# Kernel tuning notes

Measured on AMD Instinct MI355X. Metric: run time of the kernel, lower is better.

Reference implementation:

```python
import jax, jax.numpy as jnp
import numpy as np

B, T, N, D = 256, 200, 8, 64
MODEL = N * D          # 512
FFN_H = 1024 * N // 4  # 2048
EPS = 1.1920929e-07    # torch.finfo(float32).eps (nn.RMSNorm default eps=None)


def setup_inputs() -> dict:
    key = jax.random.key(0)
    ks = jax.random.split(key, 9)
    def xavier(k, shape):
        fan_in, fan_out = shape[-2], shape[-1]
        lim = float(np.sqrt(6.0 / (fan_in + fan_out)))
        return jax.random.uniform(k, shape, jnp.float32, -lim, lim)
    q = jax.random.normal(ks[0], (B, N, D), jnp.float32)
    seq = jax.random.normal(ks[1], (B, T, MODEL), jnp.float32)
    seq_mask = jax.random.randint(ks[2], (B, T), 0, 2) > 0
    seq_mask = seq_mask.at[:, 0].set(True)  # ensure >=1 valid position per row
    return {
        "q": q,
        "seq": seq,
        "rms_w": jnp.ones((MODEL,), jnp.float32),
        "w1": xavier(ks[3], (MODEL, FFN_H)),
        "w2": xavier(ks[4], (MODEL, FFN_H)),
        "w3": xavier(ks[5], (FFN_H, MODEL)),
        "w_k": xavier(ks[6], (N, D, D)),
        "w_v": xavier(ks[7], (N, D, D)),
        "seq_mask": seq_mask,
    }


def reference(q, seq, rms_w, w1, w2, w3, w_k, w_v, seq_mask):
    # RMSNorm
    sn = seq * jax.lax.rsqrt(jnp.mean(seq * seq, axis=-1, keepdims=True) + EPS) * rms_w
    # SwiGLU FFN + residual (dropout=0 / eval)
    h = (jax.nn.silu(sn @ w1) * (sn @ w2)) @ w3 + seq  # (B,T,N*D)
    hh = h.reshape(B, T, N, D)
    keys = jnp.einsum('btnd,nde->bnte', hh, w_k)    # (B,N,T,D)
    values = jnp.einsum('btnd,nde->bnte', hh, w_v)  # (B,N,T,D)
    scale = D ** (-0.5)
    scores = jnp.einsum('bnd,bntd->bnt', q, keys) * scale  # single-query attention
    scores = jnp.where(seq_mask[:, None, :], scores, -jnp.inf)
    attn = jax.nn.softmax(scores, axis=-1)
    ctx = jnp.einsum('bnt,bntd->bnd', attn, values)
    return ctx + q
```

## Files before the change

kernel.cpp:

```cpp
#include <hip/hip_runtime.h>
#include <hip/hip_fp16.h>
#include <cstdint>
#include <cstddef>

typedef unsigned short u16t;
typedef __bf16 bf16x8 __attribute__((ext_vector_type(8)));
typedef float f32x4 __attribute__((ext_vector_type(4)));
typedef unsigned short u16x8 __attribute__((ext_vector_type(8)));

#define BT_ROWS 51200
#define MODEL 512
#define FFNH 2048

__device__ __forceinline__ float bf2f(u16t u) {
  union { unsigned int i; float f; } v; v.i = ((unsigned int)u) << 16; return v.f;
}
__device__ __forceinline__ u16t f2bf(float f) {
  union { float f; unsigned int i; } v; v.f = f;
  return (u16t)((v.i + 0x7fffu + ((v.i >> 16) & 1u)) >> 16);
}
__device__ __forceinline__ float ldf(const void* p, size_t i, int dt) {
  if (dt == 1) return ((const float*)p)[i];
  u16t u = ((const u16t*)p)[i];
  if (dt == 0) return bf2f(u);
  __half h; *(u16t*)&h = u; return __half2float(h);
}
__device__ __forceinline__ void stf(void* p, size_t i, int dt, float f) {
  if (dt == 1) { ((float*)p)[i] = f; }
  else if (dt == 0) { ((u16t*)p)[i] = f2bf(f); }
  else { __half h = __float2half(f); ((u16t*)p)[i] = *(u16t*)&h; }
}
__device__ __forceinline__ void gl2lds16(const void* g, void* l) {
  __builtin_amdgcn_global_load_lds((const __attribute__((address_space(1))) void*)g,
                                   (__attribute__((address_space(3))) void*)l, 16, 0, 0);
}

__global__ __launch_bounds__(256) void detect_dtype_k(const unsigned int* __restrict__ w1,
                                                      int* __restrict__ dflag) {
  __shared__ int sh[8];
  int a = 0, bc = 0;
  for (int it = 0; it < 64; it++) {
    unsigned int w = w1[it * 256 + threadIdx.x];
    u16t lo = (u16t)(w & 0xffffu), hi = (u16t)(w >> 16);
    float flo = bf2f(lo);
    a += (!(fabsf(flo) < 0.25f)) ? 1 : 0;
    __half hh; *(u16t*)&hh = hi; float fhi = __half2float(hh);
    bc += (fabsf(fhi) > 0.25f && fabsf(fhi) < 256.f) ? 1 : 0;
  }
#pragma unroll
  for (int o = 32; o; o >>= 1) { a += __shfl_xor(a, o); bc += __shfl_xor(bc, o); }
  int w = threadIdx.x >> 6;
  if ((threadIdx.x & 63) == 0) { sh[w] = a; sh[4 + w] = bc; }
  __syncthreads();
  if (threadIdx.x == 0) {
    int A = sh[0] + sh[1] + sh[2] + sh[3];
    int B = sh[4] + sh[5] + sh[6] + sh[7];
    dflag[0] = (A > 256) ? 1 : ((B < 256) ? 2 : 0);
  }
}

__global__ __launch_bounds__(256) void detect_mask_k(const unsigned int* __restrict__ msk,
                                                     int* __restrict__ flag) {
  int i = blockIdx.x * 256 + threadIdx.x;
  int bad = 0;
  if (i < 12800) bad = (msk[i] > 1u) ? 1 : 0;
  unsigned long long bl = __ballot(bad);
  if ((threadIdx.x & 63) == 0 && bl) atomicOr(flag, 1);
}

__global__ __launch_bounds__(256) void rmsnorm_k(const void* __restrict__ seq,
                                                 const void* __restrict__ w,
                                                 const int* __restrict__ dfp,
                                                 u16t* __restrict__ xn) {
  const int dt = dfp[0];
  int row = blockIdx.x * 4 + (threadIdx.x >> 6);
  int lane = threadIdx.x & 63;
  size_t base = (size_t)row * MODEL + lane * 8;
  float x[8]; float ss = 0.f;
  if (dt == 0) {
    u16x8 xv = *(const u16x8*)((const u16t*)seq + base);
#pragma unroll
    for (int j = 0; j < 8; j++) { x[j] = bf2f(xv[j]); ss += x[j] * x[j]; }
  } else if (dt == 1) {
    const f32x4* p = (const f32x4*)((const float*)seq + base);
    f32x4 va = p[0], vb = p[1];
#pragma unroll
    for (int j = 0; j < 4; j++) { x[j] = va[j]; x[4 + j] = vb[j]; }
#pragma unroll
    for (int j = 0; j < 8; j++) ss += x[j] * x[j];
  } else {
#pragma unroll
    for (int j = 0; j < 8; j++) { x[j] = ldf(seq, base + j, dt); ss += x[j] * x[j]; }
  }
#pragma unroll
  for (int o = 32; o; o >>= 1) ss += __shfl_xor(ss, o);
  float rstd = rsqrtf(ss * (1.f / 512.f) + 1.1920929e-07f);
  u16x8 ov;
#pragma unroll
  for (int j = 0; j < 8; j++) ov[j] = f2bf(x[j] * rstd * ldf(w, lane * 8 + j, dt));
  *(u16x8*)(xn + base) = ov;
}

__global__ __launch_bounds__(256) void transpose_k(const void* __restrict__ src,
                                                   u16t* __restrict__ dst,
                                                   const int* __restrict__ dfp,
                                                   int R, int C, int ih) {
  const int dt = dfp[0];
  __shared__ u16t tile[32][33];
  int x = threadIdx.x & 31, y = threadIdx.x >> 5;
  int c0 = blockIdx.x * 32, r0 = blockIdx.y * 32;
#pragma unroll
  for (int i = 0; i < 32; i += 8)
    tile[y + i][x] = f2bf(ldf(src, (size_t)(r0 + y + i) * C + c0 + x, dt));
  __syncthreads();
#pragma unroll
  for (int i = 0; i < 32; i += 8) {
    int n = c0 + y + i;
    int vr = (ih >= 0) ? (((n >> 4) << 5) + ih * 16 + (n & 15)) : n;
    dst[(size_t)vr * R + r0 + x] = tile[x][y + i];
  }
}


#define FENCE_BAR()                              \
  do {                                           \
    __builtin_amdgcn_sched_barrier(0);           \
    __builtin_amdgcn_s_barrier();                \
    __builtin_amdgcn_sched_barrier(0);           \
  } while (0)

#define MM16(afr, bfr, MHc, NHc)                                                    \
  do {                                                                              \
    __builtin_amdgcn_s_setprio(1);                                                  \
    _Pragma("unroll") for (int ks_ = 0; ks_ < 2; ks_++)                             \
        _Pragma("unroll") for (int mi_ = 0; mi_ < 4; mi_++)                         \
            _Pragma("unroll") for (int ni_ = 0; ni_ < 2; ni_++)                     \
                acc[(MHc)*4 + mi_][(NHc)*2 + ni_] =                                 \
                    __builtin_amdgcn_mfma_f32_16x16x32_bf16(                        \
                        afr[mi_][ks_], bfr[ni_][ks_],                               \
                        acc[(MHc)*4 + mi_][(NHc)*2 + ni_], 0, 0, 0);                \
    __builtin_amdgcn_s_setprio(0);                                                  \
  } while (0)

template <int K>
__device__ __forceinline__ void gemm256_core(const u16t* __restrict__ Ag,
                                             const u16t* __restrict__ Bg,
                                             u16t* __restrict__ As,
                                             u16t* __restrict__ Bs,
                                             f32x4 (&acc)[8][4]) {
  constexpr int NKT = K / 64;
  const int tid = threadIdx.x;
  const int lane = tid & 63;
  const int wave = tid >> 6;
  const int wr = wave >> 2, wc = wave & 3;
  const int quad = lane >> 4, l16 = lane & 15;
  const int wu = tid & ~63;

  auto stage = [&](const u16t* __restrict__ G, u16t* __restrict__ L, int s, int h) {
#pragma unroll
    for (int c = 0; c < 2; c++) {
      int chunk = c * 512 + tid;
      int r = chunk >> 3;
      int k8 = (chunk & 7) ^ (r & 7);
      gl2lds16(G + (size_t)(h * 128 + r) * K + s * 64 + k8 * 8,
               L + (s & 1) * 16384 + h * 8192 + (size_t)(c * 512 + wu) * 8);
    }
  };
  auto lda = [&](bf16x8(&a)[4][2], int u, int MH) {
    const u16t* S = As + (u & 1) * 16384;
#pragma unroll
    for (int ks = 0; ks < 2; ks++)
#pragma unroll
      for (int mi = 0; mi < 4; mi++) {
        int row = wr * 128 + MH * 64 + mi * 16 + l16;
        int sw = (ks * 4 + quad) ^ (row & 7);
        a[mi][ks] = *(const bf16x8*)(S + row * 64 + sw * 8);
      }
  };
  auto ldb = [&](bf16x8(&b)[2][2], int u, int NH) {
    const u16t* S = Bs + (u & 1) * 16384;
#pragma unroll
    for (int ks = 0; ks < 2; ks++)
#pragma unroll
      for (int ni = 0; ni < 2; ni++) {
        int row = wc * 64 + NH * 32 + ni * 16 + l16;
        int sw = (ks * 4 + quad) ^ (row & 7);
        b[ni][ks] = *(const bf16x8*)(S + row * 64 + sw * 8);
      }
  };

  bf16x8 a[4][2], b0[2][2], b1[2][2];

  stage(Ag, As, 0, 0);
  stage(Ag, As, 0, 1);
  stage(Bg, Bs, 0, 0);
  stage(Bg, Bs, 0, 1);
  if (NKT > 1) stage(Ag, As, 1, 0);
  __builtin_amdgcn_sched_barrier(0);
  if (NKT > 1) asm volatile("s_waitcnt vmcnt(2)" ::: "memory");
  else         asm volatile("s_waitcnt vmcnt(0)" ::: "memory");
  __builtin_amdgcn_s_barrier();
  __builtin_amdgcn_sched_barrier(0);

  for (int u = 0; u < NKT; u++) {
    lda(a, u, 0);
    ldb(b0, u, 0);
    if (u + 1 < NKT) stage(Ag, As, u + 1, 1);
    FENCE_BAR();
    MM16(a, b0, 0, 0);
    FENCE_BAR();
    ldb(b1, u, 1);
    if (u + 1 < NKT) stage(Bg, Bs, u + 1, 0);
    FENCE_BAR();
    MM16(a, b1, 0, 1);
    FENCE_BAR();
    lda(a, u, 1);
    if (u + 1 < NKT) stage(Bg, Bs, u + 1, 1);
    FENCE_BAR();
    MM16(a, b0, 1, 0);
    FENCE_BAR();
    if (u + 2 < NKT) stage(Ag, As, u + 2, 0);
    FENCE_BAR();
    MM16(a, b1, 1, 1);
    __builtin_amdgcn_sched_barrier(0);
    if (u < NKT - 2)       asm volatile("s_waitcnt vmcnt(2)" ::: "memory");
    else if (u == NKT - 2) asm volatile("s_waitcnt vmcnt(0)" ::: "memory");
    __builtin_amdgcn_s_barrier();
    __builtin_amdgcn_sched_barrier(0);
  }
}

__device__ __forceinline__ int xcd_swz(int o, int nwg) {
  int q = nwg >> 3, r = nwg & 7;
  int xcd = o & 7, i = o >> 3;
  return (xcd < r ? xcd * (q + 1) : r * (q + 1) + (xcd - r) * q) + i;
}

__global__ __launch_bounds__(512, 2) void ffn_gemm1(const u16t* __restrict__ Xn,
                                                    const u16t* __restrict__ W12t,
                                                    u16t* __restrict__ Act) {
  __shared__ u16t As[2 * 16384];
  __shared__ u16t Bs[2 * 16384];
  const int tid = threadIdx.x;
  const int lane = tid & 63;
  const int wave = tid >> 6;
  const int wr = wave >> 2, wc = wave & 3;
  const int quad = lane >> 4, l16 = lane & 15;

  int o = blockIdx.y * 16 + blockIdx.x;
  int s = xcd_swz(o, gridDim.y * 16);
  int bx = s & 15, by = s >> 4;

  f32x4 acc[8][4];
  const f32x4 zf = {0.f, 0.f, 0.f, 0.f};
#pragma unroll
  for (int m = 0; m < 8; m++)
#pragma unroll
    for (int n = 0; n < 4; n++) acc[m][n] = zf;

  gemm256_core<512>(Xn + (size_t)by * 256 * 512, W12t + (size_t)bx * 256 * 512, As, Bs, acc);

  const int mBase = by * 256;
#pragma unroll
  for (int mi = 0; mi < 8; mi++)
#pragma unroll
    for (int p = 0; p < 2; p++)
#pragma unroll
      for (int r = 0; r < 4; r++) {
        int row = mBase + wr * 128 + mi * 16 + quad * 4 + r;
        int col = bx * 128 + (wc * 2 + p) * 16 + l16;
        float g1 = acc[mi][2 * p][r], g2 = acc[mi][2 * p + 1][r];
        float sl = g1 / (1.f + __expf(-g1));
        Act[(size_t)row * FFNH + col] = f2bf(sl * g2);
      }
}

__global__ __launch_bounds__(512, 2) void ffn_gemm2(const u16t* __restrict__ Act,
                                                    const u16t* __restrict__ W3t,
                                                    const void* __restrict__ Seq,
                                                    const int* __restrict__ dfp,
                                                    u16t* __restrict__ H, int rowOff) {
  __shared__ u16t As[2 * 16384];
  __shared__ u16t Bs[2 * 16384];
  const int dt = dfp[0];
  const int tid = threadIdx.x;
  const int lane = tid & 63;
  const int wave = tid >> 6;
  const int wr = wave >> 2, wc = wave & 3;
  const int quad = lane >> 4, l16 = lane & 15;

  int o = blockIdx.y * 2 + blockIdx.x;
  int s = xcd_swz(o, gridDim.y * 2);
  int bx = s & 1, by = s >> 1;

  f32x4 acc[8][4];
  const f32x4 zf = {0.f, 0.f, 0.f, 0.f};
#pragma unroll
  for (int m = 0; m < 8; m++)
#pragma unroll
    for (int n = 0; n < 4; n++) acc[m][n] = zf;

  gemm256_core<2048>(Act + (size_t)by * 256 * 2048, W3t + (size_t)bx * 256 * 2048, As, Bs, acc);

  const int mBase = by * 256;
#pragma unroll
  for (int mi = 0; mi < 8; mi++)
#pragma unroll
    for (int ni = 0; ni < 4; ni++)
#pragma unroll
      for (int r = 0; r < 4; r++) {
        int grow = rowOff + mBase + wr * 128 + mi * 16 + quad * 4 + r;
        int col = bx * 256 + wc * 64 + ni * 16 + l16;
        float v = acc[mi][ni][r] + ldf(Seq, (size_t)grow * MODEL + col, dt);
        H[(size_t)grow * MODEL + col] = f2bf(v);
      }
}

__global__ __launch_bounds__(256) void attn_k(const u16t* __restrict__ H,
                                              const void* __restrict__ q,
                                              const void* __restrict__ wk,
                                              const void* __restrict__ wv,
                                              const int* __restrict__ mask,
                                              const int* __restrict__ mflagp,
                                              const int* __restrict__ dfp,
                                              void* __restrict__ out) {
  const int b = blockIdx.x >> 3;
  const int n = blockIdx.x & 7;
  const int tid = threadIdx.x;
  const int w = tid >> 6;
  const int lane = tid & 63;
  const int T = 200;
  const int HS = 66;
  const int dt = dfp[0];
  const int mflag = mflagp[0];

  __shared__ u16t hbuf[200 * HS];
  __shared__ float qk[64];
  __shared__ float sc[200];
  __shared__ float part[256];
  __shared__ float red[8];
  __shared__ float ctx[64];

  for (int chunk = tid; chunk < 1600; chunk += 256) {
    int r = chunk >> 3, c = (chunk & 7) << 3;
    u16x8 v = *(const u16x8*)(H + (size_t)(b * 200 + r) * MODEL + n * 64 + c);
#pragma unroll
    for (int j = 0; j < 8; j++) hbuf[r * HS + c + j] = v[j];
  }

  {
    int d = tid >> 2, sub = tid & 3;
    float s = 0.f;
    size_t wb = ((size_t)n * 64 + d) * 64 + sub * 16;
    size_t qb = (size_t)(b * 8 + n) * 64 + sub * 16;
#pragma unroll
    for (int i = 0; i < 16; i++) s += ldf(wk, wb + i, dt) * ldf(q, qb + i, dt);
    part[tid] = s;
  }
  __syncthreads();
  if (tid < 64) qk[tid] = part[tid * 4] + part[tid * 4 + 1] + part[tid * 4 + 2] + part[tid * 4 + 3];
  __syncthreads();

  float sv = -INFINITY;
  if (tid < T) {
    float s = 0.f;
#pragma unroll 16
    for (int d = 0; d < 64; d++) s += bf2f(hbuf[tid * HS + d]) * qk[d];
    int mv = mflag ? (int)((const unsigned char*)mask)[b * 200 + tid] : mask[b * 200 + tid];
    sv = mv ? s * 0.125f : -INFINITY;
  }

  float mx = sv;
#pragma unroll
  for (int o = 32; o; o >>= 1) mx = fmaxf(mx, __shfl_xor(mx, o));
  if (lane == 0) red[w] = mx;
  __syncthreads();
  float gmax = fmaxf(fmaxf(red[0], red[1]), fmaxf(red[2], red[3]));
  float e = 0.f;
  if (gmax == -INFINITY) {
    if (tid == 0) e = 1.f;
  } else if (tid < T) {
    e = __expf(sv - gmax);
  }
  float s = e;
#pragma unroll
  for (int o = 32; o; o >>= 1) s += __shfl_xor(s, o);
  if (lane == 0) red[4 + w] = s;
  __syncthreads();
  float inv = 1.f / (red[4] + red[5] + red[6] + red[7]);
  if (tid < T) sc[tid] = e * inv;
  __syncthreads();

  float a2 = 0.f;
  for (int t = w; t < T; t += 4) a2 += sc[t] * bf2f(hbuf[t * HS + lane]);
  part[tid] = a2;
  __syncthreads();
  if (tid < 64) ctx[tid] = part[tid] + part[64 + tid] + part[128 + tid] + part[192 + tid];
  __syncthreads();

  {
    int od = tid & 63;
    float s2 = 0.f;
#pragma unroll
    for (int i = 0; i < 16; i++) {
      int d = w * 16 + i;
      s2 += ctx[d] * ldf(wv, ((size_t)n * 64 + d) * 64 + od, dt);
    }
    part[tid] = s2;
  }
  __syncthreads();
  if (tid < 64) {
    size_t oi = (size_t)(b * 8 + n) * 64 + tid;
    stf(out, oi, dt,
        part[tid] + part[64 + tid] + part[128 + tid] + part[192 + tid] + ldf(q, oi, dt));
  }
}

extern "C" void kernel_launch(void* const* d_in, const int* in_sizes, int n_in,
                              void* d_out, int out_size, void* d_ws, size_t ws_size,
                              hipStream_t stream) {
  (void)in_sizes; (void)n_in; (void)out_size;
  const void* q   = d_in[0];
  const void* seq = d_in[1];
  const void* rw  = d_in[2];
  const void* w1  = d_in[3];
  const void* w2  = d_in[4];
  const void* w3  = d_in[5];
  const void* wk  = d_in[6];
  const void* wv  = d_in[7];
  const int*  msk = (const int*)d_in[8];

  char* ws = (char*)d_ws;
  size_t off = 0;
  auto alloc = [&](size_t b) { void* p = ws + off; off = (off + b + 255) & ~(size_t)255; return p; };
  int*  flags = (int*)alloc(512);
  int*  mflag = flags + 0;
  int*  dflag = flags + 4;
  u16t* Xn   = (u16t*)alloc((size_t)BT_ROWS * MODEL * 2);
  u16t* W12t = (u16t*)alloc((size_t)2 * FFNH * MODEL * 2);
  u16t* W3t  = (u16t*)alloc((size_t)MODEL * FFNH * 2);
  size_t actBytes = (ws_size > off) ? (ws_size - off) : 0;
  long ppc = (long)(actBytes / ((size_t)256 * FFNH * 2));
  if (ppc < 1) ppc = 1;
  if (ppc > 100) ppc = 100;
  u16t* ActB = (u16t*)(ws + off);

  hipMemsetAsync(flags, 0, 512, stream);
  detect_dtype_k<<<dim3(1), dim3(256), 0, stream>>>((const unsigned int*)w1, dflag);
  detect_mask_k<<<dim3(50), dim3(256), 0, stream>>>((const unsigned int*)msk, mflag);

  rmsnorm_k<<<dim3(BT_ROWS / 4), dim3(256), 0, stream>>>(seq, rw, dflag, Xn);
  transpose_k<<<dim3(FFNH / 32, MODEL / 32), dim3(256), 0, stream>>>(w1, W12t, dflag, MODEL, FFNH, 0);
  transpose_k<<<dim3(FFNH / 32, MODEL / 32), dim3(256), 0, stream>>>(w2, W12t, dflag, MODEL, FFNH, 1);
  transpose_k<<<dim3(MODEL / 32, FFNH / 32), dim3(256), 0, stream>>>(w3, W3t, dflag, FFNH, MODEL, -1);

  for (int p0 = 0; p0 < 200; p0 += (int)ppc) {
    int panels = (200 - p0 < (int)ppc) ? (200 - p0) : (int)ppc;
    int rows0 = p0 * 256;
    ffn_gemm1<<<dim3(16, panels), dim3(512), 0, stream>>>(
        Xn + (size_t)rows0 * MODEL, W12t, ActB);
    ffn_gemm2<<<dim3(2, panels), dim3(512), 0, stream>>>(
        ActB, W3t, seq, dflag, Xn, rows0);
  }
  attn_k<<<dim3(2048), dim3(256), 0, stream>>>(Xn, q, wk, wv, msk, mflag, dflag, d_out);
}
```

Baseline: 774.7 us.

## Stage whole next K-tile up front and use nontemporal epilogue stores

Replaces the interleaved half-tile staging schedule in the GEMM core with a single issue of the full next K-tile (A and B) at the start of each iteration, followed by a full vmcnt(0) wait at the end. The sched_barrier fences around the mid-iteration barriers are dropped, leaving plain s_barriers. Epilogue stores of the activation and the H output become nontemporal to reduce cache pollution. The simpler schedule removes the finer-grained overlap of loads with MFMAs and waits for all loads each step, and without the sched fences the compiler may move LDS reads across barriers.

Measured after the change: 909.2 us. 1.17x slower.

```diff
diff --git a/kernel.cpp b/kernel.cpp
--- a/kernel.cpp
+++ b/kernel.cpp
@@ -121,13 +121,6 @@
   }
 }
 
-
-#define FENCE_BAR()                              \
-  do {                                           \
-    __builtin_amdgcn_sched_barrier(0);           \
-    __builtin_amdgcn_s_barrier();                \
-    __builtin_amdgcn_sched_barrier(0);           \
-  } while (0)
 
 #define MM16(afr, bfr, MHc, NHc)                                                    \
   do {                                                                              \
@@ -156,14 +149,16 @@
   const int quad = lane >> 4, l16 = lane & 15;
   const int wu = tid & ~63;
 
-  auto stage = [&](const u16t* __restrict__ G, u16t* __restrict__ L, int s, int h) {
-#pragma unroll
-    for (int c = 0; c < 2; c++) {
+  auto stageTile = [&](int s) {
+    u16t* Ad = As + (s & 1) * 16384;
+    u16t* Bd = Bs + (s & 1) * 16384;
+#pragma unroll
+    for (int c = 0; c < 4; c++) {
       int chunk = c * 512 + tid;
       int r = chunk >> 3;
       int k8 = (chunk & 7) ^ (r & 7);
-      gl2lds16(G + (size_t)(h * 128 + r) * K + s * 64 + k8 * 8,
-               L + (s & 1) * 16384 + h * 8192 + (size_t)(c * 512 + wu) * 8);
+      gl2lds16(Ag + (size_t)r * K + s * 64 + k8 * 8, Ad + (size_t)(c * 512 + wu) * 8);
+      gl2lds16(Bg + (size_t)r * K + s * 64 + k8 * 8, Bd + (size_t)(c * 512 + wu) * 8);
     }
   };
   auto lda = [&](bf16x8(&a)[4][2], int u, int MH) {
@@ -191,42 +186,34 @@
 
   bf16x8 a[4][2], b0[2][2], b1[2][2];
 
-  stage(Ag, As, 0, 0);
-  stage(Ag, As, 0, 1);
-  stage(Bg, Bs, 0, 0);
-  stage(Bg, Bs, 0, 1);
-  if (NKT > 1) stage(Ag, As, 1, 0);
+  stageTile(0);
   __builtin_amdgcn_sched_barrier(0);
-  if (NKT > 1) asm volatile("s_waitcnt vmcnt(2)" ::: "memory");
-  else         asm volatile("s_waitcnt vmcnt(0)" ::: "memory");
+  asm volatile("s_waitcnt vmcnt(0)" ::: "memory");
   __builtin_amdgcn_s_barrier();
   __builtin_amdgcn_sched_barrier(0);
 
   for (int u = 0; u < NKT; u++) {
+    if (u + 1 < NKT) stageTile(u + 1);
     lda(a, u, 0);
     ldb(b0, u, 0);
-    if (u + 1 < NKT) stage(Ag, As, u + 1, 1);
-    FENCE_BAR();
+    __builtin_amdgcn_s_barrier();
     MM16(a, b0, 0, 0);
-    FENCE_BAR();
+    __builtin_amdgcn_s_barrier();
     ldb(b1, u, 1);
-    if (u + 1 < NKT) stage(Bg, Bs, u + 1, 0);
-    FENCE_BAR();
+    __builtin_amdgcn_s_barrier();
     MM16(a, b1, 0, 1);
-    FENCE_BAR();
+    __builtin_amdgcn_s_barrier();
     lda(a, u, 1);
-    if (u + 1 < NKT) stage(Bg, Bs, u + 1, 1);
-    FENCE_BAR();
+    __builtin_amdgcn_s_barrier();
     MM16(a, b0, 1, 0);
-    FENCE_BAR();
-    if (u + 2 < NKT) stage(Ag, As, u + 2, 0);
-    FENCE_BAR();
+    __builtin_amdgcn_s_barrier();
     MM16(a, b1, 1, 1);
-    __builtin_amdgcn_sched_barrier(0);
-    if (u < NKT - 2)       asm volatile("s_waitcnt vmcnt(2)" ::: "memory");
-    else if (u == NKT - 2) asm volatile("s_waitcnt vmcnt(0)" ::: "memory");
-    __builtin_amdgcn_s_barrier();
-    __builtin_amdgcn_sched_barrier(0);
+    if (u + 1 < NKT) {
+      __builtin_amdgcn_sched_barrier(0);
+      asm volatile("s_waitcnt vmcnt(0)" ::: "memory");
+      __builtin_amdgcn_s_barrier();
+      __builtin_amdgcn_sched_barrier(0);
+    }
   }
 }
 
@@ -271,7 +258,7 @@
         int col = bx * 128 + (wc * 2 + p) * 16 + l16;
         float g1 = acc[mi][2 * p][r], g2 = acc[mi][2 * p + 1][r];
         float sl = g1 / (1.f + __expf(-g1));
-        Act[(size_t)row * FFNH + col] = f2bf(sl * g2);
+        __builtin_nontemporal_store(f2bf(sl * g2), &Act[(size_t)row * FFNH + col]);
       }
 }
 
@@ -312,7 +299,7 @@
         int grow = rowOff + mBase + wr * 128 + mi * 16 + quad * 4 + r;
         int col = bx * 256 + wc * 64 + ni * 16 + l16;
         float v = acc[mi][ni][r] + ldf(Seq, (size_t)grow * MODEL + col, dt);
-        H[(size_t)grow * MODEL + col] = f2bf(v);
+        __builtin_nontemporal_store(f2bf(v), &H[(size_t)grow * MODEL + col]);
       }
 }
 
```
